# Optimization experiments

Hardware: AMD Instinct MI355X
Metric: run time of the kernel (lower is better)

## Reference

```python
import jax, jax.numpy as jnp
import numpy as np

NEG_SLOPE = 0.2  # PyG GATConv default leaky_relu slope
BN_EPS = 1e-5


def gat_conv(x_src, x_dst, src, dst, w_src, w_dst, att_src, att_dst, bias):
    """Bipartite PyG GATConv, heads=H, concat=False (mean over heads), add_self_loops=True.
    x_src: [Ns, F], x_dst: [Nd, F]; src/dst: [E] int edge index; w_*: [F, H*C]; att_*: [H, C]; bias: [C].
    """
    H, C = att_src.shape
    n_dst = x_dst.shape[0]
    hs = (x_src @ w_src).reshape(-1, H, C)            # [Ns, H, C]
    hd = (x_dst @ w_dst).reshape(-1, H, C)            # [Nd, H, C]
    a_s = (hs * att_src[None]).sum(-1)                # [Ns, H]
    a_d = (hd * att_dst[None]).sum(-1)                # [Nd, H]
    # PyG adds self loops with num_nodes = min(Ns, Nd) for bipartite inputs
    n_loop = min(x_src.shape[0], n_dst)
    loop = jnp.arange(n_loop, dtype=src.dtype)
    src = jnp.concatenate([src, loop])
    dst = jnp.concatenate([dst, loop])
    e = jax.nn.leaky_relu(a_s[src] + a_d[dst], NEG_SLOPE)           # [E+L, H]
    m = jax.ops.segment_max(e, dst, num_segments=n_dst)             # [Nd, H]
    ex = jnp.exp(e - m[dst])
    den = jax.ops.segment_sum(ex, dst, num_segments=n_dst)
    alpha = ex / (den[dst] + 1e-16)                                 # neighborhood softmax
    msg = hs[src] * alpha[:, :, None]                               # [E+L, H, C]
    out = jax.ops.segment_sum(msg, dst, num_segments=n_dst)         # [Nd, H, C]
    return out.mean(axis=1) + bias


def _forward(user_ids, ingredient_ids, recipe_x, ing_src, ing_dst, ub_src, ub_dst,
             user_table, ing_table, W_rl, b_rl, bn_gamma, bn_beta,
             g1_ws, g1_wd, g1_as, g1_ad, g1_b,
             g2_ws, g2_wd, g2_as, g2_ad, g2_b):
    # nn.Embedding(max_norm=1.0): renorm looked-up rows to L2 norm <= 1
    u = user_table[user_ids]
    un = jnp.linalg.norm(u, axis=-1, keepdims=True)
    u = u * jnp.where(un > 1.0, 1.0 / (un + 1e-7), 1.0)
    # static ingredient embedding lookup
    ing = ing_table[ingredient_ids]
    # recipe linear + BatchNorm (training-mode batch stats; dropout off = eval)
    r = recipe_x @ W_rl + b_rl
    mu = r.mean(axis=0)
    var = ((r - mu) ** 2).mean(axis=0)
    r = bn_gamma * (r - mu) * jax.lax.rsqrt(var + BN_EPS) + bn_beta
    # ingredient -> recipe GAT, residual add
    r = r + gat_conv(ing, r, ing_src, ing_dst, g1_ws, g1_wd, g1_as, g1_ad, g1_b)
    # user -> recipe GAT
    r = gat_conv(u, r, ub_src, ub_dst, g2_ws, g2_wd, g2_as, g2_ad, g2_b)
    return r


def setup_inputs() -> dict:
    key = jax.random.key(0)
    ks = jax.random.split(key, 24)
    NU, NR, NI = 50000, 100000, 20000
    D_IN, H, C = 20, 2, 128
    E1, E2 = 400000, 800000
    s = 0.05
    f32 = jnp.float32
    inp = {
        "user_ids": jax.random.randint(ks[0], (NU,), 0, NU, dtype=jnp.int32),
        "ingredient_ids": jax.random.randint(ks[1], (NI,), 0, NI, dtype=jnp.int32),
        "recipe_x": jax.random.normal(ks[2], (NR, D_IN), f32),
        "ing_src": jax.random.randint(ks[3], (E1,), 0, NI, dtype=jnp.int32),
        "ing_dst": jax.random.randint(ks[4], (E1,), 0, NR, dtype=jnp.int32),
        "ub_src": jax.random.randint(ks[5], (E2,), 0, NU, dtype=jnp.int32),
        "ub_dst": jax.random.randint(ks[6], (E2,), 0, NR, dtype=jnp.int32),
        "user_table": jax.random.normal(ks[7], (NU, C), f32) * s,
        "ing_table": jax.random.normal(ks[8], (NI, C), f32) * s,
        "W_rl": jax.random.normal(ks[9], (D_IN, C), f32) * s,
        "b_rl": jnp.zeros((C,), f32),
        "bn_gamma": jnp.ones((C,), f32),
        "bn_beta": jnp.zeros((C,), f32),
        "g1_ws": jax.random.normal(ks[10], (C, H * C), f32) * s,
        "g1_wd": jax.random.normal(ks[11], (C, H * C), f32) * s,
        "g1_as": jax.random.normal(ks[12], (H, C), f32) * s,
        "g1_ad": jax.random.normal(ks[13], (H, C), f32) * s,
        "g1_b": jnp.zeros((C,), f32),
        "g2_ws": jax.random.normal(ks[14], (C, H * C), f32) * s,
        "g2_wd": jax.random.normal(ks[15], (C, H * C), f32) * s,
        "g2_as": jax.random.normal(ks[16], (H, C), f32) * s,
        "g2_ad": jax.random.normal(ks[17], (H, C), f32) * s,
        "g2_b": jnp.zeros((C,), f32),
    }
    return inp


def reference(user_ids, ingredient_ids, recipe_x, ing_src, ing_dst, ub_src, ub_dst,
              user_table, ing_table, W_rl, b_rl, bn_gamma, bn_beta,
              g1_ws, g1_wd, g1_as, g1_ad, g1_b,
              g2_ws, g2_wd, g2_as, g2_ad, g2_b):
    return _forward(user_ids, ingredient_ids, recipe_x, ing_src, ing_dst, ub_src, ub_dst,
                    user_table, ing_table, W_rl, b_rl, bn_gamma, bn_beta,
                    g1_ws, g1_wd, g1_as, g1_ad, g1_b,
                    g2_ws, g2_wd, g2_as, g2_ad, g2_b)
```

## Files before the change

### kernel.cpp

```cpp
#include <hip/hip_runtime.h>
#include <hip/hip_bf16.h>
#include <math.h>

#define DIN 20
#define C 128
#define HC 256
#define EB2 2048
#define MAXNB 400
#define CAP 8192
#define CAPSH 13

typedef unsigned short u16;
typedef unsigned int u32;
typedef unsigned long long u64;
typedef __bf16 bf16x8 __attribute__((ext_vector_type(8)));
typedef float f32x4 __attribute__((ext_vector_type(4)));

__device__ __forceinline__ float bfbits2f(unsigned int lo16) {
    return __uint_as_float(lo16 << 16);
}
__device__ __forceinline__ u16 f2bf_rne(float f) {
    unsigned int b = __float_as_uint(f);
    return (u16)((b + 0x7FFFu + ((b >> 16) & 1u)) >> 16);
}

__device__ __forceinline__ void scan512f(u32* cnt, u32* off, u32* wsum4) {
    int t = threadIdx.x;
    int l = t & 63, w = t >> 6;
    u32 a = cnt[2 * t], b = cnt[2 * t + 1];
    u32 s = a + b;
    u32 isc = s;
    #pragma unroll
    for (int o = 1; o < 64; o <<= 1) {
        u32 n = __shfl_up(isc, o);
        if (l >= o) isc += n;
    }
    if (l == 63) wsum4[w] = isc;
    __syncthreads();
    u32 pre = 0;
    if (w > 0) pre += wsum4[0];
    if (w > 1) pre += wsum4[1];
    if (w > 2) pre += wsum4[2];
    u32 excl = pre + isc - s;
    off[2 * t] = excl;
    off[2 * t + 1] = excl + a;
    __syncthreads();
}

__device__ __forceinline__ void edge_at(int i, const int* s1, const int* d1,
    const int* s2, const int* d2, int E1, int T1, int E2, int NR,
    int& s, int& key)
{
    if (i < T1) {
        if (i < E1) { s = s1[i]; key = d1[i]; }
        else        { s = i - E1; key = i - E1; }
    } else {
        int k = i - T1;
        if (k < E2) { s = s2[k]; key = NR + d2[k]; }
        else        { s = k - E2; key = NR + (k - E2); }
    }
}

__global__ __launch_bounds__(256) void k_init(const float* __restrict__ x, int NR,
    float* __restrict__ stats, int SB, int A2B,
    const int* __restrict__ src1, const int* __restrict__ dst1,
    const int* __restrict__ src2, const int* __restrict__ dst2,
    int E1, int L1, int E2, int L2, int NB,
    u32* __restrict__ bucketFill, u32* __restrict__ pairs,
    const float* __restrict__ g2_ws, u16* __restrict__ wsp,
    const float* __restrict__ g1_wd, const float* __restrict__ g1_ad,
    const float* __restrict__ g2_wd, const float* __restrict__ g2_ad,
    const float* __restrict__ g1_ws, const float* __restrict__ g1_as,
    const float* __restrict__ g2_as, const float* __restrict__ g1b)
{
    __shared__ __align__(16) char sm[40528];
    int t = threadIdx.x;
    int bid = blockIdx.x;
    if (bid < SB) {
        float (*L)[DIN] = (float(*)[DIN])sm;
        int r = bid * 256 + t;
        if (r < NR) {
            const float4* xp = (const float4*)(x + (size_t)r * DIN);
            float4 v0 = xp[0], v1 = xp[1], v2 = xp[2], v3 = xp[3], v4 = xp[4];
            L[t][0] = v0.x; L[t][1] = v0.y; L[t][2] = v0.z; L[t][3] = v0.w;
            L[t][4] = v1.x; L[t][5] = v1.y; L[t][6] = v1.z; L[t][7] = v1.w;
            L[t][8] = v2.x; L[t][9] = v2.y; L[t][10] = v2.z; L[t][11] = v2.w;
            L[t][12] = v3.x; L[t][13] = v3.y; L[t][14] = v3.z; L[t][15] = v3.w;
            L[t][16] = v4.x; L[t][17] = v4.y; L[t][18] = v4.z; L[t][19] = v4.w;
        } else {
            #pragma unroll
            for (int k = 0; k < DIN; k++) L[t][k] = 0.f;
        }
        __syncthreads();
        if (t < 210) {
            int p = 0, q = t;
            while (q >= DIN - p) { q -= (DIN - p); p++; }
            q += p;
            float acc = 0.f;
            for (int rr = 0; rr < 256; rr++) acc += L[rr][p] * L[rr][q];
            atomicAdd(&stats[p * DIN + q], acc);
            if (p != q) atomicAdd(&stats[q * DIN + p], acc);
        } else if (t < 230) {
            int k = t - 210;
            float acc = 0.f;
            for (int rr = 0; rr < 256; rr++) acc += L[rr][k];
            atomicAdd(&stats[400 + k], acc);
        }
        return;
    }
    if (bid < SB + A2B) {
        u64* ldsE = (u64*)sm;
        u64* ldsS = ldsE + EB2;
        u32* cntA = (u32*)(ldsS + EB2);
        u32* cntB = cntA + 512;
        u32* offL = cntB + 512;
        u32* wsum4 = offL + 512;
        u32* gbase = wsum4 + 4;
        for (int i = t; i < 512; i += 256) { cntA[i] = 0; cntB[i] = 0; }
        __syncthreads();
        int T1 = E1 + L1, T = T1 + E2 + L2;
        int base = (bid - SB) * EB2;
        int nE = T - base; if (nE > EB2) nE = EB2;
        for (int j = t; j < nE; j += 256) {
            int s, key;
            edge_at(base + j, src1, dst1, src2, dst2, E1, T1, E2, NR, s, key);
            ldsE[j] = ((u64)(u32)key << 32) | (u32)s;
            atomicAdd(&cntA[key >> 9], 1u);
        }
        __syncthreads();
        scan512f(cntA, offL, wsum4);
        for (int b = t; b < NB; b += 256) {
            u32 c = cntA[b];
            gbase[b] = c ? (((u32)b << CAPSH) + atomicAdd(&bucketFill[b], c)) : 0u;
        }
        __syncthreads();
        for (int j = t; j < nE; j += 256) {
            u64 e = ldsE[j];
            u32 b = ((u32)(e >> 32)) >> 9;
            u32 r = atomicAdd(&cntB[b], 1u);
            ldsS[offL[b] + r] = e;
        }
        __syncthreads();
        for (int j = t; j < nE; j += 256) {
            u64 e = ldsS[j];
            u32 key = (u32)(e >> 32);
            u32 b = key >> 9;
            pairs[gbase[b] + ((u32)j - offL[b])] = ((key & 511u) << 17) | (u32)e;
        }
        return;
    }
    if (bid < SB + A2B + 32) {
        int idx0 = ((bid - SB - A2B) * 256 + t) * 4;
        #pragma unroll
        for (int i = 0; i < 4; i++) {
            int flat = idx0 + i;
            int j = flat & 7;
            int lane = (flat >> 3) & 63;
            int kb = (flat >> 9) & 3;
            int nt = flat >> 11;
            int k = kb * 32 + (lane >> 4) * 8 + j;
            int n = nt * 16 + (lane & 15);
            wsp[flat] = f2bf_rne(g2_ws[k * HC + n]);
        }
        return;
    }
    int dr = bid - SB - A2B - 32;
    const float* wm = (dr == 0) ? g1_wd : (dr == 1) ? g2_wd : (dr == 2) ? g1_ws : g2_ws;
    const float* am = (dr == 0) ? g1_ad : (dr == 1) ? g2_ad : (dr == 2) ? g1_as : g2_as;
    int obase = (dr == 0) ? 676 : (dr == 1) ? 932 : (dr == 2) ? 1200 : 1456;
    float* vd2l = (float*)sm;
    float acc = 0.f;
    {
        int k = t >> 1, h = t & 1;
        const float4* wp = (const float4*)(wm + k * HC + h * C);
        const float4* ap = (const float4*)(am + h * C);
        #pragma unroll 4
        for (int q = 0; q < 32; q++) {
            float4 xv = wp[q], yv = ap[q];
            acc += xv.x * yv.x + xv.y * yv.y + xv.z * yv.z + xv.w * yv.w;
        }
        stats[obase + t] = acc;
    }
    if (dr == 1) {
        vd2l[t] = acc;
        __syncthreads();
        int k = t >> 1, h = t & 1;
        const float4* ws1p = (const float4*)(g1_ws + k * HC + h * C);
        float t0 = 0.f, t1 = 0.f;
        #pragma unroll 4
        for (int q = 0; q < 32; q++) {
            float4 wv = ws1p[q];
            int c = q * 4;
            t0 += wv.x * vd2l[(c + 0) * 2 + 0] + wv.y * vd2l[(c + 1) * 2 + 0]
                + wv.z * vd2l[(c + 2) * 2 + 0] + wv.w * vd2l[(c + 3) * 2 + 0];
            t1 += wv.x * vd2l[(c + 0) * 2 + 1] + wv.y * vd2l[(c + 1) * 2 + 1]
                + wv.z * vd2l[(c + 2) * 2 + 1] + wv.w * vd2l[(c + 3) * 2 + 1];
        }
        stats[1712 + t * 2 + 0] = t0;
        stats[1712 + t * 2 + 1] = t1;
        if (t < 2) {
            float cb = 0.f;
            for (int k2 = 0; k2 < C; k2++) cb += g1b[k2] * vd2l[k2 * 2 + t];
            stats[1188 + t] = cb;
        }
    }
}

__global__ __launch_bounds__(256) void k_fin(const u32* __restrict__ pairs,
    const u32* __restrict__ bucketFill, int n2, int NB, int R0B, int IB,
    int* __restrict__ off2, int* __restrict__ sorted,
    const float* __restrict__ x, int NR, const float* __restrict__ stats,
    const float* __restrict__ W, const float* __restrict__ gamma,
    const float* __restrict__ beta, float invN,
    float* __restrict__ a_d, float* __restrict__ advd,
    const float* __restrict__ ing_table, const int* __restrict__ ing_ids, int NI,
    float* __restrict__ a_si, float* __restrict__ psi,
    const float* __restrict__ user_table, const int* __restrict__ user_ids, int NU,
    const u16* __restrict__ wsp, u16* __restrict__ hs16, float* __restrict__ a_su)
{
    __shared__ __align__(16) char sm[30736];
    int t = threadIdx.x;
    int bid = blockIdx.x;
    if (bid < NB) {
        u32* cntA = (u32*)sm;
        u32* cntB = cntA + 512;
        u32* offL = cntB + 512;
        u32* wsum4 = offL + 512;
        u32* ldsS = wsum4 + 4;
        int b = bid;
        u32 beg = (u32)b << CAPSH;
        u32 fill = bucketFill[b];
        u32 end = beg + fill;
        int dstBase = b << 9;
        for (int i = t; i < 512; i += 256) { cntA[i] = 0; cntB[i] = 0; }
        __syncthreads();
        for (u32 j = beg + t; j < end; j += 256) {
            u32 fine = pairs[j] >> 17;
            atomicAdd(&cntA[fine], 1u);
        }
        __syncthreads();
        scan512f(cntA, offL, wsum4);
        for (int d = t; d < 512; d += 256) {
            int gk = dstBase + d;
            if (gk < n2) {
                int s0 = (int)(beg + offL[d]);
                off2[2 * gk] = s0;
                off2[2 * gk + 1] = s0 + (int)cntA[d];
            }
        }
        bool fast = fill <= 6144u;
        __syncthreads();
        for (u32 j = beg + t; j < end; j += 256) {
            u32 p = pairs[j];
            u32 d = p >> 17;
            u32 r = atomicAdd(&cntB[d], 1u);
            u32 pos = offL[d] + r;
            u32 src = p & 0x1FFFFu;
            if (fast) ldsS[pos] = src;
            else sorted[beg + pos] = (int)src;
        }
        __syncthreads();
        if (fast) {
            for (u32 j = t; j < fill; j += 256) sorted[beg + j] = (int)ldsS[j];
        }
        return;
    }
    if (bid < NB + R0B) {
        float* Sm   = (float*)sm;
        float* Wm   = Sm + 420;
        float* vd1s = Wm + 2560;
        float* vd2s = vd1s + 256;
        float* sS   = vd2s + 256;
        float* sSh  = sS + 128;
        float* fv   = sSh + 128;
        for (int i = t; i < 420; i += 256) Sm[i] = stats[i];
        for (int i = t; i < DIN * C; i += 256) Wm[i] = W[i];
        vd1s[t] = stats[676 + t];
        vd2s[t] = stats[932 + t];
        __syncthreads();
        if (t < C) {
            float w[DIN];
            #pragma unroll
            for (int k = 0; k < DIN; k++) w[k] = Wm[k * C + t];
            float mb = 0.f;
            #pragma unroll
            for (int k = 0; k < DIN; k++) mb += Sm[400 + k] * invN * w[k];
            float e2 = 0.f;
            for (int p = 0; p < DIN; p++) {
                float acc2 = 0.f;
                #pragma unroll
                for (int q = 0; q < DIN; q++) acc2 += Sm[p * DIN + q] * w[q];
                e2 += w[p] * acc2;
            }
            e2 *= invN;
            float var = e2 - mb * mb;
            float s = gamma[t] * rsqrtf(var + 1e-5f);
            sS[t] = s;
            sSh[t] = beta[t] - s * mb;
        }
        __syncthreads();
        if (t < 80) {
            int k = t >> 2, h4 = t & 3, h = h4 & 1;
            const float* vs = (h4 < 2) ? vd1s : vd2s;
            float acc = 0.f;
            for (int c = 0; c < C; c++) acc += sS[c] * Wm[k * C + c] * vs[c * 2 + h];
            fv[t] = acc;
        } else if (t < 84) {
            int h4 = t - 80, h = h4 & 1;
            const float* vs = (h4 < 2) ? vd1s : vd2s;
            float acc = 0.f;
            for (int c = 0; c < C; c++) acc += sSh[c] * vs[c * 2 + h];
            fv[t] = acc;
        }
        __syncthreads();
        int r = (bid - NB) * 256 + t;
        if (r < NR) {
            const float4* xp = (const float4*)(x + (size_t)r * DIN);
            float4 v0 = xp[0], v1 = xp[1], v2 = xp[2], v3 = xp[3], v4 = xp[4];
            float xv[20] = {v0.x, v0.y, v0.z, v0.w, v1.x, v1.y, v1.z, v1.w,
                            v2.x, v2.y, v2.z, v2.w, v3.x, v3.y, v3.z, v3.w,
                            v4.x, v4.y, v4.z, v4.w};
            float a0 = 0.f, a1 = 0.f, b0 = 0.f, b1 = 0.f;
            #pragma unroll
            for (int k = 0; k < DIN; k++) {
                float xvk = xv[k];
                a0 += xvk * fv[k * 4 + 0];
                a1 += xvk * fv[k * 4 + 1];
                b0 += xvk * fv[k * 4 + 2];
                b1 += xvk * fv[k * 4 + 3];
            }
            ((float2*)a_d)[r]  = make_float2(a0 + fv[80], a1 + fv[81]);
            ((float2*)advd)[r] = make_float2(b0 + fv[82], b1 + fv[83]);
        }
        return;
    }
    if (bid < NB + R0B + IB) {
        float* u1s = (float*)sm;
        float* Ts  = u1s + 256;
        u1s[t] = stats[1200 + t];
        Ts[t] = stats[1712 + t];
        Ts[256 + t] = stats[1968 + t];
        __syncthreads();
        int r = t >> 3, cg = t & 7;
        int row = (bid - NB - R0B) * 32 + r;
        float as0 = 0.f, as1 = 0.f, p00 = 0.f, p01 = 0.f, p10 = 0.f, p11 = 0.f;
        if (row < NI) {
            const float* xp = ing_table + (size_t)ing_ids[row] * C + cg * 16;
            #pragma unroll
            for (int q = 0; q < 4; q++) {
                float4 v = ((const float4*)xp)[q];
                float xvv[4] = {v.x, v.y, v.z, v.w};
                #pragma unroll
                for (int jj = 0; jj < 4; jj++) {
                    int k = cg * 16 + q * 4 + jj;
                    float xx = xvv[jj];
                    as0 += xx * u1s[k * 2 + 0];
                    as1 += xx * u1s[k * 2 + 1];
                    p00 += xx * Ts[k * 4 + 0];
                    p01 += xx * Ts[k * 4 + 1];
                    p10 += xx * Ts[k * 4 + 2];
                    p11 += xx * Ts[k * 4 + 3];
                }
            }
        }
        #pragma unroll
        for (int m = 1; m <= 4; m <<= 1) {
            as0 += __shfl_xor(as0, m); as1 += __shfl_xor(as1, m);
            p00 += __shfl_xor(p00, m); p01 += __shfl_xor(p01, m);
            p10 += __shfl_xor(p10, m); p11 += __shfl_xor(p11, m);
        }
        if (cg == 0 && row < NI) {
            ((float2*)a_si)[row] = make_float2(as0, as1);
            float4 pv; pv.x = p00; pv.y = p01; pv.z = p10; pv.w = p11;
            ((float4*)psi)[row] = pv;
        }
        return;
    }
    u16* A = (u16*)sm;
    float* u2s = (float*)(sm + 8704);
    u2s[t] = stats[1456 + t];
    int rowBase = (bid - NB - R0B - IB) * 32;
    int r = t >> 3, cg = t & 7;
    int row = rowBase + r;
    float xv[16];
    if (row < NU) {
        const float* xp = user_table + (size_t)user_ids[row] * C + cg * 16;
        #pragma unroll
        for (int q = 0; q < 4; q++) {
            float4 v = ((const float4*)xp)[q];
            xv[q * 4 + 0] = v.x; xv[q * 4 + 1] = v.y;
            xv[q * 4 + 2] = v.z; xv[q * 4 + 3] = v.w;
        }
    } else {
        #pragma unroll
        for (int q = 0; q < 16; q++) xv[q] = 0.f;
    }
    float ss = 0.f;
    #pragma unroll
    for (int q = 0; q < 16; q++) ss += xv[q] * xv[q];
    #pragma unroll
    for (int m = 1; m <= 4; m <<= 1) ss += __shfl_xor(ss, m);
    float nn = sqrtf(ss);
    float f = (nn > 1.f) ? 1.f / (nn + 1e-7f) : 1.f;
    float as0 = 0.f, as1 = 0.f;
    #pragma unroll
    for (int q = 0; q < 16; q++) {
        xv[q] *= f;
        int k = cg * 16 + q;
        as0 += xv[q] * u2s[k * 2 + 0];
        as1 += xv[q] * u2s[k * 2 + 1];
    }
    #pragma unroll
    for (int m = 1; m <= 4; m <<= 1) {
        as0 += __shfl_xor(as0, m); as1 += __shfl_xor(as1, m);
    }
    if (cg == 0 && row < NU) ((float2*)a_su)[row] = make_float2(as0, as1);
    {
        union { u16 h[16]; uint4 u4[2]; } pk;
        #pragma unroll
        for (int q = 0; q < 16; q++) pk.h[q] = f2bf_rne(xv[q]);
        uint4* dst = (uint4*)&A[r * 136 + cg * 16];
        dst[0] = pk.u4[0];
        dst[1] = pk.u4[1];
    }
    __syncthreads();
    int w = t >> 6, l = t & 63;
    int m15 = l & 15, q4 = l >> 4;
    bf16x8 afrag[2][4];
    #pragma unroll
    for (int mt = 0; mt < 2; mt++)
        #pragma unroll
        for (int kb = 0; kb < 4; kb++)
            afrag[mt][kb] = *(const bf16x8*)&A[(mt * 16 + m15) * 136 + kb * 32 + q4 * 8];
    f32x4 acc[2][4];
    #pragma unroll
    for (int mt = 0; mt < 2; mt++)
        #pragma unroll
        for (int i = 0; i < 4; i++) acc[mt][i] = (f32x4){0.f, 0.f, 0.f, 0.f};
    #pragma unroll
    for (int kb = 0; kb < 4; kb++) {
        #pragma unroll
        for (int i = 0; i < 4; i++) {
            int nt = w * 4 + i;
            bf16x8 bfrag = *(const bf16x8*)&wsp[((nt * 4 + kb) * 64 + l) * 8];
            acc[0][i] = __builtin_amdgcn_mfma_f32_16x16x32_bf16(afrag[0][kb], bfrag, acc[0][i], 0, 0, 0);
            acc[1][i] = __builtin_amdgcn_mfma_f32_16x16x32_bf16(afrag[1][kb], bfrag, acc[1][i], 0, 0, 0);
        }
    }
    #pragma unroll
    for (int mt = 0; mt < 2; mt++) {
        #pragma unroll
        for (int i = 0; i < 4; i++) {
            int col = (w * 4 + i) * 16 + m15;
            #pragma unroll
            for (int rr = 0; rr < 4; rr++) {
                int rw = rowBase + mt * 16 + q4 * 4 + rr;
                if (rw < NU) hs16[(size_t)rw * HC + col] = f2bf_rne(acc[mt][i][rr]);
            }
        }
    }
}

__global__ __launch_bounds__(256) void k_agg(const int* __restrict__ off2, const int* __restrict__ sorted,
    const float* __restrict__ a_si, const float* __restrict__ psi,
    const float* __restrict__ a_d1, const float* __restrict__ advd,
    const float* __restrict__ cb,
    const float* __restrict__ a_su, const u16* __restrict__ hs16,
    const float* __restrict__ bias, int NR, float* __restrict__ out)
{
    int wave = threadIdx.x >> 6, lane = threadIdx.x & 63;
    int d = blockIdx.x * 4 + wave;
    if (d >= NR) return;
    int beg = off2[2 * d], end = off2[2 * d + 1];
    float ad0 = a_d1[d * 2 + 0], ad1 = a_d1[d * 2 + 1];
    float w0s = 0.f, w1s = 0.f, a00 = 0.f, a01 = 0.f, a10 = 0.f, a11 = 0.f;
    for (int j = beg + lane; j < end; j += 64) {
        int s = sorted[j];
        float2 as = ((const float2*)a_si)[s];
        float e0 = as.x + ad0; e0 = (e0 >= 0.f) ? e0 : 0.2f * e0;
        float e1 = as.y + ad1; e1 = (e1 >= 0.f) ? e1 : 0.2f * e1;
        float x0 = __expf(e0), x1 = __expf(e1);
        float4 p = ((const float4*)psi)[s];
        w0s += x0; w1s += x1;
        a00 += x0 * p.x; a01 += x0 * p.y;
        a10 += x1 * p.z; a11 += x1 * p.w;
    }
    #pragma unroll
    for (int o = 1; o < 64; o <<= 1) {
        w0s += __shfl_xor(w0s, o); w1s += __shfl_xor(w1s, o);
        a00 += __shfl_xor(a00, o); a01 += __shfl_xor(a01, o);
        a10 += __shfl_xor(a10, o); a11 += __shfl_xor(a11, o);
    }
    float inv0g = 1.f / (w0s + 1e-16f), inv1g = 1.f / (w1s + 1e-16f);
    float r0 = advd[d * 2 + 0] + cb[0] + 0.5f * (a00 * inv0g + a10 * inv1g);
    float r1 = advd[d * 2 + 1] + cb[1] + 0.5f * (a01 * inv0g + a11 * inv1g);
    int i2 = NR + d;
    int beg2 = off2[2 * i2], end2 = off2[2 * i2 + 1];
    int head = lane >> 5;
    int q = lane & 31;
    u32 laneoff = (u32)(head * 256 + q * 8);
    int hsel = lane & 32;
    float adh = head ? r1 : r0;
    float wsum = 0.f;
    float acc0 = 0.f, acc1 = 0.f, acc2 = 0.f, acc3 = 0.f;
    const char* hbase = (const char*)hs16;

    for (int base = beg2; base < end2; base += 32) {
        int rem = end2 - base; if (rem > 32) rem = 32;
        int j = q; if (j >= rem) j = rem - 1;
        int sp = sorted[base + j];
        u32 boff = ((u32)sp) << 9;
        float asv = a_su[sp * 2 + head];
        float ee = asv + adh; ee = (ee >= 0.f) ? ee : 0.2f * ee;
        float wcomb = __expf(ee);
        int e = 0;
        for (; e + 4 <= rem; e += 4) {
            u32 b0 = __shfl(boff, e + 0), b1 = __shfl(boff, e + 1);
            u32 b2 = __shfl(boff, e + 2), b3 = __shfl(boff, e + 3);
            uint2 g0 = *(const uint2*)(hbase + (b0 + laneoff));
            uint2 g1 = *(const uint2*)(hbase + (b1 + laneoff));
            uint2 g2 = *(const uint2*)(hbase + (b2 + laneoff));
            uint2 g3 = *(const uint2*)(hbase + (b3 + laneoff));
            float W0 = __shfl(wcomb, hsel + e + 0);
            float W1 = __shfl(wcomb, hsel + e + 1);
            float W2 = __shfl(wcomb, hsel + e + 2);
            float W3 = __shfl(wcomb, hsel + e + 3);
            wsum += (W0 + W1) + (W2 + W3);
            acc0 += W0 * bfbits2f(g0.x & 0xFFFFu);
            acc1 += W0 * __uint_as_float(g0.x & 0xFFFF0000u);
            acc2 += W0 * bfbits2f(g0.y & 0xFFFFu);
            acc3 += W0 * __uint_as_float(g0.y & 0xFFFF0000u);
            acc0 += W1 * bfbits2f(g1.x & 0xFFFFu);
            acc1 += W1 * __uint_as_float(g1.x & 0xFFFF0000u);
            acc2 += W1 * bfbits2f(g1.y & 0xFFFFu);
            acc3 += W1 * __uint_as_float(g1.y & 0xFFFF0000u);
            acc0 += W2 * bfbits2f(g2.x & 0xFFFFu);
            acc1 += W2 * __uint_as_float(g2.x & 0xFFFF0000u);
            acc2 += W2 * bfbits2f(g2.y & 0xFFFFu);
            acc3 += W2 * __uint_as_float(g2.y & 0xFFFF0000u);
            acc0 += W3 * bfbits2f(g3.x & 0xFFFFu);
            acc1 += W3 * __uint_as_float(g3.x & 0xFFFF0000u);
            acc2 += W3 * bfbits2f(g3.y & 0xFFFFu);
            acc3 += W3 * __uint_as_float(g3.y & 0xFFFF0000u);
        }
        for (; e < rem; e++) {
            u32 b0 = __shfl(boff, e);
            float W = __shfl(wcomb, hsel + e);
            uint2 g = *(const uint2*)(hbase + (b0 + laneoff));
            wsum += W;
            acc0 += W * bfbits2f(g.x & 0xFFFFu);
            acc1 += W * __uint_as_float(g.x & 0xFFFF0000u);
            acc2 += W * bfbits2f(g.y & 0xFFFFu);
            acc3 += W * __uint_as_float(g.y & 0xFFFF0000u);
        }
    }
    float inv = 1.f / (wsum + 1e-16f);
    float v0 = acc0 * inv, v1 = acc1 * inv, v2 = acc2 * inv, v3 = acc3 * inv;
    v0 = 0.5f * (v0 + __shfl_xor(v0, 32));
    v1 = 0.5f * (v1 + __shfl_xor(v1, 32));
    v2 = 0.5f * (v2 + __shfl_xor(v2, 32));
    v3 = 0.5f * (v3 + __shfl_xor(v3, 32));
    if (lane < 32) {
        float4 bb = ((const float4*)bias)[q];
        float4 o;
        o.x = v0 + bb.x; o.y = v1 + bb.y; o.z = v2 + bb.z; o.w = v3 + bb.w;
        ((float4*)(out + (size_t)d * C))[q] = o;
    }
}

extern "C" void kernel_launch(void* const* d_in, const int* in_sizes, int n_in,
                              void* d_out, int out_size, void* d_ws, size_t ws_size,
                              hipStream_t stream) {
    const int*   user_ids       = (const int*)d_in[0];
    const int*   ingredient_ids = (const int*)d_in[1];
    const float* recipe_x       = (const float*)d_in[2];
    const int*   ing_src        = (const int*)d_in[3];
    const int*   ing_dst        = (const int*)d_in[4];
    const int*   ub_src         = (const int*)d_in[5];
    const int*   ub_dst         = (const int*)d_in[6];
    const float* user_table     = (const float*)d_in[7];
    const float* ing_table      = (const float*)d_in[8];
    const float* W_rl           = (const float*)d_in[9];
    const float* bn_gamma       = (const float*)d_in[11];
    const float* bn_beta        = (const float*)d_in[12];
    const float* g1_ws          = (const float*)d_in[13];
    const float* g1_wd          = (const float*)d_in[14];
    const float* g1_as          = (const float*)d_in[15];
    const float* g1_ad          = (const float*)d_in[16];
    const float* g1_b           = (const float*)d_in[17];
    const float* g2_ws          = (const float*)d_in[18];
    const float* g2_wd          = (const float*)d_in[19];
    const float* g2_as          = (const float*)d_in[20];
    const float* g2_ad          = (const float*)d_in[21];
    const float* g2_b           = (const float*)d_in[22];

    int NU = in_sizes[0];
    int NI = in_sizes[1];
    int NR = in_sizes[2] / DIN;
    int E1 = in_sizes[3];
    int E2 = in_sizes[5];
    int Nmax = (NI > NU) ? NI : NU;
    int L1 = (NI < NR) ? NI : NR;
    int L2 = (NU < NR) ? NU : NR;
    int Etot = E1 + L1 + E2 + L2;
    int n2 = 2 * NR;
    int NB = (n2 + 511) >> 9;

    char* w = (char*)d_ws;
    u16*   hs16  = (u16*)w;    w += (size_t)Nmax * HC * 2;
    float* a_si  = (float*)w;  w += (size_t)NI * 2 * 4;
    float* a_su  = (float*)w;  w += (size_t)NU * 2 * 4;
    float* psi   = (float*)w;  w += (size_t)NI * 4 * 4;
    float* a_d   = (float*)w;  w += (size_t)NR * 2 * 4;
    float* advd  = (float*)w;  w += (size_t)NR * 2 * 4;
    float* stats = (float*)w;  w += 2432 * 4;
    u32*   bucketFill = (u32*)w; w += MAXNB * 4;
    u16*   wsp   = (u16*)w;    w += 32768 * 2;
    int*   off2  = (int*)w;    w += (size_t)(2 * n2) * 4;
    int*   sorted= (int*)w;    w += (size_t)NB * CAP * 4;
    u32*   pairs = (u32*)w;    w += (size_t)NB * CAP * 4;

    hipMemsetAsync(stats, 0, (2432 + MAXNB) * 4, stream);

    int SB  = (NR + 255) / 256;
    int A2B = (Etot + EB2 - 1) / EB2;
    k_init<<<SB + A2B + 32 + 4, 256, 0, stream>>>(recipe_x, NR, stats, SB, A2B,
                                              ing_src, ing_dst, ub_src, ub_dst,
                                              E1, L1, E2, L2, NB,
                                              bucketFill, pairs, g2_ws, wsp,
                                              g1_wd, g1_ad, g2_wd, g2_ad,
                                              g1_ws, g1_as, g2_as, g1_b);
    int R0B = (NR + 255) / 256;
    int IB  = (NI + 31) / 32;
    int HB  = (NU + 31) / 32;
    k_fin<<<NB + R0B + IB + HB, 256, 0, stream>>>(pairs, bucketFill, n2, NB, R0B, IB,
                                                  off2, sorted,
                                                  recipe_x, NR, stats,
                                                  W_rl, bn_gamma, bn_beta, 1.0f / NR,
                                                  a_d, advd,
                                                  ing_table, ingredient_ids, NI, a_si, psi,
                                                  user_table, user_ids, NU,
                                                  wsp, hs16, a_su);
    k_agg<<<(NR + 3) / 4, 256, 0, stream>>>(off2, sorted, a_si, psi, a_d, advd,
                                            stats + 1188, a_su, hs16, g2_b, NR,
                                            (float*)d_out);
}
```

Before: 292.1 us.

## Process two destination nodes per wave with half-wave groups and 16-byte gathers

The aggregation kernel now maps two destination recipes to each 64-lane wave, one per 32-lane half, instead of one recipe per wave. Each lane gathers 16 bytes (8 bf16 values) per neighbour row instead of 8. This halves the block count and gives each load more width, aiming to reduce idle lanes on low-degree nodes and issue fewer, wider memory requests. The cost is a fully serial inner loop without the previous 4-way unroll, more registers per lane, and extra shuffles per edge.

```diff
diff --git a/kernel.cpp b/kernel.cpp
--- a/kernel.cpp
+++ b/kernel.cpp
@@ -469,12 +469,16 @@
     const float* __restrict__ bias, int NR, float* __restrict__ out)
 {
     int wave = threadIdx.x >> 6, lane = threadIdx.x & 63;
-    int d = blockIdx.x * 4 + wave;
-    if (d >= NR) return;
-    int beg = off2[2 * d], end = off2[2 * d + 1];
-    float ad0 = a_d1[d * 2 + 0], ad1 = a_d1[d * 2 + 1];
+    int g = lane >> 5, lg = lane & 31;
+    int d = blockIdx.x * 8 + wave * 2 + g;
+    bool dv = d < NR;
+    int dd = dv ? d : NR - 1;
+    int sbase = lane & 32;
+    int beg = off2[2 * dd];
+    int end = dv ? off2[2 * dd + 1] : beg;
+    float ad0 = a_d1[dd * 2 + 0], ad1 = a_d1[dd * 2 + 1];
     float w0s = 0.f, w1s = 0.f, a00 = 0.f, a01 = 0.f, a10 = 0.f, a11 = 0.f;
-    for (int j = beg + lane; j < end; j += 64) {
+    for (int j = beg + lg; j < end; j += 32) {
         int s = sorted[j];
         float2 as = ((const float2*)a_si)[s];
         float e0 = as.x + ad0; e0 = (e0 >= 0.f) ? e0 : 0.2f * e0;
@@ -486,85 +490,68 @@
         a10 += x1 * p.z; a11 += x1 * p.w;
     }
     #pragma unroll
-    for (int o = 1; o < 64; o <<= 1) {
+    for (int o = 1; o < 32; o <<= 1) {
         w0s += __shfl_xor(w0s, o); w1s += __shfl_xor(w1s, o);
         a00 += __shfl_xor(a00, o); a01 += __shfl_xor(a01, o);
         a10 += __shfl_xor(a10, o); a11 += __shfl_xor(a11, o);
     }
     float inv0g = 1.f / (w0s + 1e-16f), inv1g = 1.f / (w1s + 1e-16f);
-    float r0 = advd[d * 2 + 0] + cb[0] + 0.5f * (a00 * inv0g + a10 * inv1g);
-    float r1 = advd[d * 2 + 1] + cb[1] + 0.5f * (a01 * inv0g + a11 * inv1g);
-    int i2 = NR + d;
-    int beg2 = off2[2 * i2], end2 = off2[2 * i2 + 1];
-    int head = lane >> 5;
-    int q = lane & 31;
-    u32 laneoff = (u32)(head * 256 + q * 8);
-    int hsel = lane & 32;
-    float adh = head ? r1 : r0;
+    float r0 = advd[dd * 2 + 0] + cb[0] + 0.5f * (a00 * inv0g + a10 * inv1g);
+    float r1 = advd[dd * 2 + 1] + cb[1] + 0.5f * (a01 * inv0g + a11 * inv1g);
+    int i2 = NR + dd;
+    int beg2 = off2[2 * i2];
+    int end2 = dv ? off2[2 * i2 + 1] : beg2;
+    int head = lg >> 4, hq = lg & 15;
+    u32 laneoff = (u32)(head * 256 + hq * 16);
     float wsum = 0.f;
-    float acc0 = 0.f, acc1 = 0.f, acc2 = 0.f, acc3 = 0.f;
+    float acc[8];
+    #pragma unroll
+    for (int k = 0; k < 8; k++) acc[k] = 0.f;
     const char* hbase = (const char*)hs16;
 
     for (int base = beg2; base < end2; base += 32) {
         int rem = end2 - base; if (rem > 32) rem = 32;
-        int j = q; if (j >= rem) j = rem - 1;
+        int j = lg; if (j >= rem) j = rem - 1;
         int sp = sorted[base + j];
         u32 boff = ((u32)sp) << 9;
-        float asv = a_su[sp * 2 + head];
-        float ee = asv + adh; ee = (ee >= 0.f) ? ee : 0.2f * ee;
-        float wcomb = __expf(ee);
-        int e = 0;
-        for (; e + 4 <= rem; e += 4) {
-            u32 b0 = __shfl(boff, e + 0), b1 = __shfl(boff, e + 1);
-            u32 b2 = __shfl(boff, e + 2), b3 = __shfl(boff, e + 3);
-            uint2 g0 = *(const uint2*)(hbase + (b0 + laneoff));
-            uint2 g1 = *(const uint2*)(hbase + (b1 + laneoff));
-            uint2 g2 = *(const uint2*)(hbase + (b2 + laneoff));
-            uint2 g3 = *(const uint2*)(hbase + (b3 + laneoff));
-            float W0 = __shfl(wcomb, hsel + e + 0);
-            float W1 = __shfl(wcomb, hsel + e + 1);
-            float W2 = __shfl(wcomb, hsel + e + 2);
-            float W3 = __shfl(wcomb, hsel + e + 3);
-            wsum += (W0 + W1) + (W2 + W3);
-            acc0 += W0 * bfbits2f(g0.x & 0xFFFFu);
-            acc1 += W0 * __uint_as_float(g0.x & 0xFFFF0000u);
-            acc2 += W0 * bfbits2f(g0.y & 0xFFFFu);
-            acc3 += W0 * __uint_as_float(g0.y & 0xFFFF0000u);
-            acc0 += W1 * bfbits2f(g1.x & 0xFFFFu);
-            acc1 += W1 * __uint_as_float(g1.x & 0xFFFF0000u);
-            acc2 += W1 * bfbits2f(g1.y & 0xFFFFu);
-            acc3 += W1 * __uint_as_float(g1.y & 0xFFFF0000u);
-            acc0 += W2 * bfbits2f(g2.x & 0xFFFFu);
-            acc1 += W2 * __uint_as_float(g2.x & 0xFFFF0000u);
-            acc2 += W2 * bfbits2f(g2.y & 0xFFFFu);
-            acc3 += W2 * __uint_as_float(g2.y & 0xFFFF0000u);
-            acc0 += W3 * bfbits2f(g3.x & 0xFFFFu);
-            acc1 += W3 * __uint_as_float(g3.x & 0xFFFF0000u);
-            acc2 += W3 * bfbits2f(g3.y & 0xFFFFu);
-            acc3 += W3 * __uint_as_float(g3.y & 0xFFFF0000u);
-        }
-        for (; e < rem; e++) {
-            u32 b0 = __shfl(boff, e);
-            float W = __shfl(wcomb, hsel + e);
-            uint2 g = *(const uint2*)(hbase + (b0 + laneoff));
+        float2 av = ((const float2*)a_su)[sp];
+        float e0 = av.x + r0; e0 = (e0 >= 0.f) ? e0 : 0.2f * e0;
+        float e1 = av.y + r1; e1 = (e1 >= 0.f) ? e1 : 0.2f * e1;
+        float w0 = __expf(e0), w1 = __expf(e1);
+        for (int e = 0; e < rem; e++) {
+            int srcl = sbase + e;
+            u32 bo = __shfl(boff, srcl);
+            float W0 = __shfl(w0, srcl);
+            float W1 = __shfl(w1, srcl);
+            float W = head ? W1 : W0;
+            uint4 gg = *(const uint4*)(hbase + (bo + laneoff));
             wsum += W;
-            acc0 += W * bfbits2f(g.x & 0xFFFFu);
-            acc1 += W * __uint_as_float(g.x & 0xFFFF0000u);
-            acc2 += W * bfbits2f(g.y & 0xFFFFu);
-            acc3 += W * __uint_as_float(g.y & 0xFFFF0000u);
+            acc[0] += W * bfbits2f(gg.x & 0xFFFFu);
+            acc[1] += W * __uint_as_float(gg.x & 0xFFFF0000u);
+            acc[2] += W * bfbits2f(gg.y & 0xFFFFu);
+            acc[3] += W * __uint_as_float(gg.y & 0xFFFF0000u);
+            acc[4] += W * bfbits2f(gg.z & 0xFFFFu);
+            acc[5] += W * __uint_as_float(gg.z & 0xFFFF0000u);
+            acc[6] += W * bfbits2f(gg.w & 0xFFFFu);
+            acc[7] += W * __uint_as_float(gg.w & 0xFFFF0000u);
         }
     }
     float inv = 1.f / (wsum + 1e-16f);
-    float v0 = acc0 * inv, v1 = acc1 * inv, v2 = acc2 * inv, v3 = acc3 * inv;
-    v0 = 0.5f * (v0 + __shfl_xor(v0, 32));
-    v1 = 0.5f * (v1 + __shfl_xor(v1, 32));
-    v2 = 0.5f * (v2 + __shfl_xor(v2, 32));
-    v3 = 0.5f * (v3 + __shfl_xor(v3, 32));
-    if (lane < 32) {
-        float4 bb = ((const float4*)bias)[q];
-        float4 o;
-        o.x = v0 + bb.x; o.y = v1 + bb.y; o.z = v2 + bb.z; o.w = v3 + bb.w;
-        ((float4*)(out + (size_t)d * C))[q] = o;
+    #pragma unroll
+    for (int k = 0; k < 8; k++) {
+        float v = acc[k] * inv;
+        acc[k] = 0.5f * (v + __shfl_xor(v, 16));
+    }
+    if (dv && head == 0) {
+        const float4* b4 = (const float4*)bias;
+        float4 bb0 = b4[hq * 2], bb1 = b4[hq * 2 + 1];
+        float4 o0, o1;
+        o0.x = acc[0] + bb0.x; o0.y = acc[1] + bb0.y;
+        o0.z = acc[2] + bb0.z; o0.w = acc[3] + bb0.w;
+        o1.x = acc[4] + bb1.x; o1.y = acc[5] + bb1.y;
+        o1.z = acc[6] + bb1.z; o1.w = acc[7] + bb1.w;
+        float4* op = (float4*)(out + (size_t)d * C + hq * 8);
+        op[0] = o0; op[1] = o1;
     }
 }
 
@@ -641,7 +628,7 @@
                                                   ing_table, ingredient_ids, NI, a_si, psi,
                                                   user_table, user_ids, NU,
                                                   wsp, hs16, a_su);
-    k_agg<<<(NR + 3) / 4, 256, 0, stream>>>(off2, sorted, a_si, psi, a_d, advd,
+    k_agg<<<(NR + 7) / 8, 256, 0, stream>>>(off2, sorted, a_si, psi, a_d, advd,
                                             stats + 1188, a_su, hs16, g2_b, NR,
                                             (float*)d_out);
 }
```

After: 284.2 us (median of 2 runs). -2.7%, faster.
